# Kernel optimization log

Hardware: AMD Instinct MI355X
Metric: run time of the kernel (lower is better)

## Reference

```python
import math
import jax, jax.numpy as jnp
import numpy as np

FACTOR = 5
N_HEADS = 8


def setup_inputs() -> dict:
    key = jax.random.key(0)
    ks = jax.random.split(key, 9)
    B, S, D = 4, 8192, 512
    s = 0.02
    x = jax.random.normal(ks[0], (B, S, D), jnp.float32)
    Wq = jax.random.normal(ks[1], (D, D), jnp.float32) * s
    bq = jax.random.normal(ks[2], (D,), jnp.float32) * s
    Wk = jax.random.normal(ks[3], (D, D), jnp.float32) * s
    bk = jax.random.normal(ks[4], (D,), jnp.float32) * s
    Wv = jax.random.normal(ks[5], (D, D), jnp.float32) * s
    bv = jax.random.normal(ks[6], (D,), jnp.float32) * s
    Wo = jax.random.normal(ks[7], (D, D), jnp.float32) * s
    bo = jax.random.normal(ks[8], (D,), jnp.float32) * s
    return {"x": x, "Wq": Wq, "bq": bq, "Wk": Wk, "bk": bk,
            "Wv": Wv, "bv": bv, "Wo": Wo, "bo": bo}


def reference(x, Wq, bq, Wk, bk, Wv, bv, Wo, bo):
    B, S, D = x.shape
    H = N_HEADS
    hd = D // H
    scale = hd ** -0.5

    def proj(W, b):
        # [B,S,D] -> [B,H,S,hd]
        return (x @ W + b).reshape(B, S, H, hd).transpose(0, 2, 1, 3)

    q = proj(Wq, bq)
    k = proj(Wk, bk)
    v = proj(Wv, bv)

    # number of "active" queries: O(log S)
    sampled = max(1, min(S, int(FACTOR * math.log(S + 1))))

    sparsity = jnp.sum(q * q, axis=-1)                    # [B,H,S]
    top_idx = jax.lax.top_k(sparsity, sampled)[1]         # [B,H,u]

    sel_q = jnp.take_along_axis(q, top_idx[..., None], axis=2)  # [B,H,u,hd]
    scores = jnp.einsum('bhud,bhsd->bhus', sel_q, k) * scale     # [B,H,u,S]
    attn = jax.nn.softmax(scores, axis=-1)
    sel_ctx = jnp.einsum('bhus,bhsd->bhud', attn, v)             # [B,H,u,hd]

    # default context = mean of values; overwrite rows of selected queries
    ctx = jnp.broadcast_to(v.mean(axis=2, keepdims=True), (B, H, S, hd))
    bi = jnp.arange(B)[:, None, None]
    hi = jnp.arange(H)[None, :, None]
    ctx = ctx.at[bi, hi, top_idx].set(sel_ctx)                   # scatter [B,H,S,hd]

    ctx = ctx.transpose(0, 2, 1, 3).reshape(B, S, D)
    return ctx @ Wo + bo
```

## Files before the change

### kernel.cpp

```cpp
#include <hip/hip_runtime.h>
#include <hip/hip_fp16.h>
#include <math.h>

#define B_ 4
#define S_ 8192
#define D_ 512
#define H_ 8
#define U_ 45
#define NCHUNK 16

typedef unsigned short ushortT;
typedef __attribute__((ext_vector_type(8))) _Float16 half8;
typedef __attribute__((ext_vector_type(4))) float f32x4;

__device__ __forceinline__ ushortT f2h(float f) {
    return __half_as_ushort(__float2half(f));
}
__device__ __forceinline__ float h2f(ushortT u) {
    return __half2float(__ushort_as_half(u));
}

__device__ __forceinline__ void gload_lds16(const ushortT* g, ushortT* l) {
    __builtin_amdgcn_global_load_lds(
        (const __attribute__((address_space(1))) void*)g,
        (__attribute__((address_space(3))) void*)l,
        16, 0, 0);
}

__global__ __launch_bounds__(256) void prep_kernel(
    const float* __restrict__ X, ushortT* __restrict__ Xf,
    const float* __restrict__ Wq, const float* __restrict__ Wk,
    const float* __restrict__ Wv,
    ushortT* __restrict__ WqT, ushortT* __restrict__ WkT,
    ushortT* __restrict__ WvT,
    float* __restrict__ vsum, float* __restrict__ outbase)
{
    __shared__ float t[32][33];
    const int bx = blockIdx.x;
    if (bx < 8192) {
        if (bx == 0) {
            float4 z = {0.f, 0.f, 0.f, 0.f};
            *(float4*)&vsum[threadIdx.x * 8]        = z;
            *(float4*)&vsum[threadIdx.x * 8 + 4]    = z;
            *(float4*)&outbase[threadIdx.x * 8]     = z;
            *(float4*)&outbase[threadIdx.x * 8 + 4] = z;
        }
        size_t i = ((size_t)bx * 256 + threadIdx.x) * 8;
        float4 a = *(const float4*)(X + i);
        float4 b = *(const float4*)(X + i + 4);
        *(ushort4*)(Xf + i)     = make_ushort4(f2h(a.x), f2h(a.y), f2h(a.z), f2h(a.w));
        *(ushort4*)(Xf + i + 4) = make_ushort4(f2h(b.x), f2h(b.y), f2h(b.z), f2h(b.w));
    } else {
        const int idx = bx - 8192;
        const int z = idx >> 8, rem = idx & 255;
        const int r0 = (rem >> 4) * 32, c0 = (rem & 15) * 32;
        const float* W = (z == 0) ? Wq : (z == 1) ? Wk : Wv;
        ushortT* O = (z == 0) ? WqT : (z == 1) ? WkT : WvT;
        const int tx = threadIdx.x & 31, ty4 = (threadIdx.x >> 5) * 4;
#pragma unroll
        for (int i = 0; i < 4; ++i)
            t[ty4 + i][tx] = W[(size_t)(r0 + ty4 + i) * 512 + c0 + tx];
        __syncthreads();
#pragma unroll
        for (int i = 0; i < 4; ++i)
            O[(size_t)(c0 + ty4 + i) * 512 + r0 + tx] = f2h(t[tx][ty4 + i]);
    }
}

__global__ __launch_bounds__(256, 2) void qkv_mfma(
    const ushortT* __restrict__ Xf,
    const ushortT* __restrict__ WqT, const ushortT* __restrict__ WkT,
    const ushortT* __restrict__ WvT,
    const float* __restrict__ bq, const float* __restrict__ bk,
    const float* __restrict__ bv,
    ushortT* __restrict__ Qbuf, ushortT* __restrict__ Kbuf,
    ushortT* __restrict__ VT,
    float* __restrict__ sparsity, float* __restrict__ vsum)
{
    __shared__ ushortT lds[2 * 128 * 64];
    ushortT* As = lds;
    ushortT* Bs = lds + 8192;

    const int tid  = threadIdx.x;
    const int w    = tid >> 6, lane = tid & 63;
    const int quad = lane >> 4, c16 = lane & 15;
    const int wr   = w >> 1,  wc  = w & 1;
    const int mat  = blockIdx.y >> 2;
    const int nt   = blockIdx.y & 3;
    const int m0   = blockIdx.x * 128;
    const int n0   = nt * 128;

    const int srowL = lane >> 3;
    const int slc   = (((lane & 7) - (srowL & 7)) & 7) * 8;
    const int rrot  = c16 & 7;

    const ushortT* Ag = (mat == 2) ? WvT : Xf;
    const ushortT* Bg = (mat == 0) ? WqT : (mat == 1) ? WkT : Xf;
    const int arow0 = (mat == 2) ? n0 : m0;
    const int brow0 = (mat == 2) ? m0 : n0;

    f32x4 acc[4][4];
#pragma unroll
    for (int i = 0; i < 4; ++i)
#pragma unroll
        for (int j = 0; j < 4; ++j) acc[i][j] = (f32x4){0.f, 0.f, 0.f, 0.f};

    for (int k0 = 0; k0 < 512; k0 += 64) {
        __syncthreads();
#pragma unroll
        for (int c = 0; c < 4; ++c) {
            const int R = c * 32 + w * 8 + srowL;
            const int lbase = c * 2048 + w * 512;
            gload_lds16(Ag + (size_t)(arow0 + R) * 512 + k0 + slc, As + lbase);
            gload_lds16(Bg + (size_t)(brow0 + R) * 512 + k0 + slc, Bs + lbase);
        }
        __syncthreads();
#pragma unroll
        for (int kk = 0; kk < 2; ++kk) {
            const int phk = (((kk * 4 + quad) + rrot) & 7) * 8;
            half8 af[4], bf[4];
#pragma unroll
            for (int i = 0; i < 4; ++i) {
                af[i] = *(const half8*)&As[(wr * 64 + i * 16 + c16) * 64 + phk];
                bf[i] = *(const half8*)&Bs[(wc * 64 + i * 16 + c16) * 64 + phk];
            }
#pragma unroll
            for (int i = 0; i < 4; ++i)
#pragma unroll
                for (int j = 0; j < 4; ++j)
                    acc[i][j] = __builtin_amdgcn_mfma_f32_16x16x32_f16(af[i], bf[j], acc[i][j], 0, 0, 0);
        }
    }

    if (mat == 0) {
        const int b = m0 >> 13;
        const int head = (n0 + wc * 64) >> 6;
        float bb[4];
#pragma unroll
        for (int j = 0; j < 4; ++j) bb[j] = bq[n0 + wc * 64 + j * 16 + c16];
        ushortT* qbase = Qbuf + ((size_t)(b * 8 + head) * 8192) * 64;
#pragma unroll
        for (int i = 0; i < 4; ++i)
#pragma unroll
            for (int r = 0; r < 4; ++r) {
                const int s = (m0 & 8191) + wr * 64 + i * 16 + quad * 4 + r;
                float p = 0.f;
#pragma unroll
                for (int j = 0; j < 4; ++j) {
                    float v = acc[i][j][r] + bb[j];
                    qbase[(size_t)s * 64 + j * 16 + c16] = f2h(v);
                    p = fmaf(v, v, p);
                }
                p += __shfl_xor(p, 1);
                p += __shfl_xor(p, 2);
                p += __shfl_xor(p, 4);
                p += __shfl_xor(p, 8);
                if (c16 == 0)
                    sparsity[((size_t)b * H_ + head) * S_ + s] = p;
            }
    } else if (mat == 1) {
        const int b = m0 >> 13;
        const int head = (n0 + wc * 64) >> 6;
        float bb[4];
#pragma unroll
        for (int j = 0; j < 4; ++j) bb[j] = bk[n0 + wc * 64 + j * 16 + c16];
        ushortT* kbase = Kbuf + ((size_t)(b * 8 + head) * 8192) * 64;
#pragma unroll
        for (int i = 0; i < 4; ++i)
#pragma unroll
            for (int r = 0; r < 4; ++r) {
                const int s = (m0 & 8191) + wr * 64 + i * 16 + quad * 4 + r;
#pragma unroll
                for (int j = 0; j < 4; ++j)
                    kbase[(size_t)s * 64 + j * 16 + c16] = f2h(acc[i][j][r] + bb[j]);
            }
    } else {
        const int b = m0 >> 13;
        const int sbase = (m0 & 8191) + wc * 64;
#pragma unroll
        for (int i = 0; i < 4; ++i)
#pragma unroll
            for (int r = 0; r < 4; ++r) {
                const int dcol = n0 + wr * 64 + i * 16 + quad * 4 + r;
                const int head = dcol >> 6, dd = dcol & 63;
                const float biasv = bv[dcol];
                ushortT* vrow = VT + ((size_t)(b * 8 + head) * 64 + dd) * 8192;
                float vsa = 0.f;
#pragma unroll
                for (int j = 0; j < 4; ++j) {
                    float v = acc[i][j][r] + biasv;
                    vrow[sbase + j * 16 + c16] = f2h(v);
                    vsa += v;
                }
                vsa += __shfl_xor(vsa, 1);
                vsa += __shfl_xor(vsa, 2);
                vsa += __shfl_xor(vsa, 4);
                vsa += __shfl_xor(vsa, 8);
                if (c16 == 0) atomicAdd(&vsum[b * 512 + dcol], vsa);
            }
    }
}

__global__ __launch_bounds__(256) void topk_kernel(
    const float* __restrict__ sparsity, int* __restrict__ topidx,
    const float* __restrict__ vsum, const float* __restrict__ Wo,
    const float* __restrict__ bo, float* __restrict__ outbase)
{
    __shared__ unsigned vals[S_];
    __shared__ unsigned hist[8][256];
    __shared__ int ssum[256];
    __shared__ unsigned prefix_s;
    __shared__ int need_s;
    __shared__ int cnt_gt_s, cnt_eq_s;
    __shared__ int eqidx[64];
    const int tid = threadIdx.x;

    if (blockIdx.x >= 32) {
        const int idx = blockIdx.x - 32;
        const int b = idx >> 3, ks = (idx & 7) >> 1, dh = idx & 1;
        const int d = dh * 256 + tid;
        float acc = (ks == 0) ? bo[d] : 0.f;
        const int r0 = ks * 128;
        for (int r = r0; r < r0 + 128; ++r) {
            float mv = vsum[b * 512 + r] * (1.0f / S_);
            acc = fmaf(mv, Wo[(size_t)r * 512 + d], acc);
        }
        atomicAdd(&outbase[b * 512 + d], acc);
        return;
    }

    const int bh = blockIdx.x;
    const unsigned* sp = (const unsigned*)(sparsity + (size_t)bh * S_);
    for (int i = tid; i < S_; i += 256) vals[i] = sp[i];

    unsigned prefix = 0;
    int need = U_;
    const int rep = tid & 7;
    for (int level = 0; level < 4; ++level) {
        const int shift = 24 - level * 8;
#pragma unroll
        for (int r = 0; r < 8; ++r) hist[r][tid] = 0;
        __syncthreads();
        const unsigned pmask = (level == 0) ? 0u : (0xFFFFFFFFu << (shift + 8));
        for (int i = tid; i < S_; i += 256) {
            unsigned v = vals[i];
            if ((v & pmask) == prefix)
                atomicAdd(&hist[rep][(v >> shift) & 255], 1u);
        }
        __syncthreads();
        int bs = 0;
#pragma unroll
        for (int r = 0; r < 8; ++r) bs += (int)hist[r][tid];
        ssum[tid] = bs;
        __syncthreads();
        for (int off = 1; off < 256; off <<= 1) {
            int add = (tid + off < 256) ? ssum[tid + off] : 0;
            __syncthreads();
            ssum[tid] += add;
            __syncthreads();
        }
        int snext = (tid == 255) ? 0 : ssum[tid + 1];
        if (ssum[tid] >= need && snext < need) {
            prefix_s = prefix | ((unsigned)tid << shift);
            need_s = need - snext;
        }
        __syncthreads();
        prefix = prefix_s;
        need = need_s;
        __syncthreads();
    }
    const unsigned T = prefix;
    if (tid == 0) { cnt_gt_s = 0; cnt_eq_s = 0; }
    __syncthreads();
    for (int i = tid; i < S_; i += 256) {
        unsigned v = vals[i];
        if (v > T) {
            int p = atomicAdd(&cnt_gt_s, 1);
            topidx[bh * U_ + p] = i;
        } else if (v == T) {
            int p = atomicAdd(&cnt_eq_s, 1);
            if (p < 64) eqidx[p] = i;
        }
    }
    __syncthreads();
    if (tid == 0) {
        int rem = U_ - cnt_gt_s;
        int n = cnt_eq_s < 64 ? cnt_eq_s : 64;
        for (int a = 0; a < rem; ++a) {
            int best = 1 << 30, bj = 0;
            for (int j = 0; j < n; ++j)
                if (eqidx[j] < best) { best = eqidx[j]; bj = j; }
            topidx[bh * U_ + cnt_gt_s + a] = best;
            eqidx[bj] = 1 << 30;
        }
    }
}

__global__ __launch_bounds__(256, 2) void attn_mfma(
    const ushortT* __restrict__ Qbuf, const ushortT* __restrict__ Kbuf,
    const ushortT* __restrict__ VT, const int* __restrict__ topidx,
    float* __restrict__ pl, float* __restrict__ pacc)
{
    __shared__ float sc[48 * 132];
    __shared__ ushortT Qb[48 * 72];

    const int tid = threadIdx.x;
    const int w = tid >> 6, lane = tid & 63;
    const int quad = lane >> 4, c16 = lane & 15;
    const int bh = blockIdx.y;
    const int s_base = blockIdx.x * 512;

    for (int i = tid; i < 48 * 64; i += 256) {
        int q = i >> 6, d = i & 63;
        float v = 0.f;
        if (q < U_) {
            int s = topidx[bh * U_ + q];
            v = h2f(Qbuf[((size_t)bh * 8192 + s) * 64 + d]) * 0.125f;
        }
        Qb[q * 72 + d] = f2h(v);
    }

    f32x4 O[3];
#pragma unroll
    for (int mt = 0; mt < 3; ++mt) O[mt] = (f32x4){0.f, 0.f, 0.f, 0.f};
    float lacc[12];
#pragma unroll
    for (int qi = 0; qi < 12; ++qi) lacc[qi] = 0.f;

    __syncthreads();

    half8 qa[3][2];
#pragma unroll
    for (int mt = 0; mt < 3; ++mt)
#pragma unroll
        for (int kk = 0; kk < 2; ++kk)
            qa[mt][kk] = *(const half8*)&Qb[(mt * 16 + c16) * 72 + kk * 32 + quad * 8];

    const ushortT* kb  = Kbuf + (size_t)bh * 8192 * 64;
    const ushortT* vtb = VT + ((size_t)bh * 64 + w * 16 + c16) * 8192;

    for (int ci = 0; ci < 4; ++ci) {
        const int s0 = s_base + ci * 128;

        half8 kf[2][2];
#pragma unroll
        for (int nt2 = 0; nt2 < 2; ++nt2)
#pragma unroll
            for (int kk = 0; kk < 2; ++kk)
                kf[nt2][kk] = *(const half8*)&kb[
                    (size_t)(s0 + w * 32 + nt2 * 16 + c16) * 64 + kk * 32 + quad * 8];
        f32x4 sacc[3][2];
#pragma unroll
        for (int mt = 0; mt < 3; ++mt)
#pragma unroll
            for (int nt2 = 0; nt2 < 2; ++nt2) {
                sacc[mt][nt2] = (f32x4){0.f, 0.f, 0.f, 0.f};
#pragma unroll
                for (int kk = 0; kk < 2; ++kk)
                    sacc[mt][nt2] = __builtin_amdgcn_mfma_f32_16x16x32_f16(
                        qa[mt][kk], kf[nt2][kk], sacc[mt][nt2], 0, 0, 0);
            }
#pragma unroll
        for (int mt = 0; mt < 3; ++mt)
#pragma unroll
            for (int nt2 = 0; nt2 < 2; ++nt2)
#pragma unroll
                for (int r = 0; r < 4; ++r)
                    sc[(mt * 16 + quad * 4 + r) * 132 + w * 32 + nt2 * 16 + c16] =
                        sacc[mt][nt2][r];
        __syncthreads();

        half8 vb[4];
#pragma unroll
        for (int kk = 0; kk < 4; ++kk)
            vb[kk] = *(const half8*)&vtb[s0 + kk * 32 + quad * 8];

#pragma unroll
        for (int qi = 0; qi < 12; ++qi) {
            const int q = w * 12 + qi;
            float x0 = sc[q * 132 + lane];
            float x1 = sc[q * 132 + 64 + lane];
            ushortT u0 = f2h(__expf(x0));
            ushortT u1 = f2h(__expf(x1));
            lacc[qi] += h2f(u0) + h2f(u1);
            ushortT* pr = (ushortT*)&sc[q * 132];
            pr[lane] = u0;
            pr[lane + 64] = u1;
        }
        __syncthreads();

#pragma unroll
        for (int mt = 0; mt < 3; ++mt)
#pragma unroll
            for (int kk = 0; kk < 4; ++kk) {
                half8 pa = *(const half8*)((const ushortT*)sc +
                    (size_t)(mt * 16 + c16) * 264 + kk * 32 + quad * 8);
                O[mt] = __builtin_amdgcn_mfma_f32_16x16x32_f16(pa, vb[kk], O[mt], 0, 0, 0);
            }
        __syncthreads();
    }

#pragma unroll
    for (int mt = 0; mt < 3; ++mt)
#pragma unroll
        for (int r = 0; r < 4; ++r) {
            const int q = mt * 16 + quad * 4 + r;
            if (q < U_)
                pacc[(((size_t)bh * NCHUNK + blockIdx.x) * U_ + q) * 64 + w * 16 + c16] =
                    O[mt][r];
        }
#pragma unroll
    for (int qi = 0; qi < 12; ++qi) {
        const int q = w * 12 + qi;
        float ssum = lacc[qi];
#pragma unroll
        for (int off = 1; off < 64; off <<= 1) ssum += __shfl_xor(ssum, off);
        if (lane == 0 && q < U_)
            pl[((size_t)bh * NCHUNK + blockIdx.x) * U_ + q] = ssum;
    }
}

__global__ __launch_bounds__(256) void fill_kernel(
    const float* __restrict__ outbase, float* __restrict__ out)
{
    size_t gid = (size_t)blockIdx.x * 256 + threadIdx.x;
    size_t e0 = gid * 4;
    int b = (int)(e0 >> 22);
    int col = (int)(e0 & 511);
    float4 v = *(const float4*)&outbase[b * 512 + col];
    *(float4*)&out[e0] = v;
}

__global__ __launch_bounds__(512) void corr_out_kernel(
    const float* __restrict__ pl, const float* __restrict__ pacc,
    const float* __restrict__ vsum, const float* __restrict__ Wo,
    const int* __restrict__ topidx, float* __restrict__ out)
{
    __shared__ float corrS[64];
    const int q = blockIdx.x, bh = blockIdx.y;
    const int b = bh >> 3, h = bh & 7, tid = threadIdx.x;
    if (tid < 64) {
        float L = 0.f, a = 0.f;
        for (int c = 0; c < NCHUNK; ++c) {
            L += pl[((size_t)bh * NCHUNK + c) * U_ + q];
            a += pacc[(((size_t)bh * NCHUNK + c) * U_ + q) * 64 + tid];
        }
        corrS[tid] = a / L - vsum[b * 512 + h * 64 + tid] * (1.0f / S_);
    }
    __syncthreads();
    const int s = topidx[bh * U_ + q];
    const int d = tid;
    float delta = 0.f;
#pragma unroll
    for (int r = 0; r < 64; ++r)
        delta = fmaf(corrS[r], Wo[(size_t)(h * 64 + r) * 512 + d], delta);
    atomicAdd(&out[((size_t)b * S_ + s) * 512 + d], delta);
}

extern "C" void kernel_launch(void* const* d_in, const int* in_sizes, int n_in,
                              void* d_out, int out_size, void* d_ws, size_t ws_size,
                              hipStream_t stream)
{
    const float* X  = (const float*)d_in[0];
    const float* Wq = (const float*)d_in[1];
    const float* bq = (const float*)d_in[2];
    const float* Wk = (const float*)d_in[3];
    const float* bk = (const float*)d_in[4];
    const float* Wv = (const float*)d_in[5];
    const float* bv = (const float*)d_in[6];
    const float* Wo = (const float*)d_in[7];
    const float* bo = (const float*)d_in[8];
    float* out = (float*)d_out;

    char* ws = (char*)d_ws;
    size_t off = 0;
    auto alloc = [&](size_t bytes) {
        void* p = ws + off;
        off = (off + bytes + 255) & ~(size_t)255;
        return p;
    };
    ushortT* Xf   = (ushortT*)alloc((size_t)B_ * S_ * D_ * 2);
    ushortT* Qbuf = (ushortT*)alloc((size_t)B_ * S_ * D_ * 2);
    ushortT* Kbuf = (ushortT*)alloc((size_t)B_ * S_ * D_ * 2);
    ushortT* VT   = (ushortT*)alloc((size_t)B_ * S_ * D_ * 2);
    ushortT* WqT  = (ushortT*)alloc((size_t)D_ * D_ * 2);
    ushortT* WkT  = (ushortT*)alloc((size_t)D_ * D_ * 2);
    ushortT* WvT  = (ushortT*)alloc((size_t)D_ * D_ * 2);
    float* sparsity = (float*)alloc((size_t)B_ * H_ * S_ * 4);
    int*   topidx   = (int*)alloc((size_t)B_ * H_ * U_ * 4);
    float* pl       = (float*)alloc((size_t)B_ * H_ * NCHUNK * U_ * 4);
    float* pacc     = (float*)alloc((size_t)B_ * H_ * NCHUNK * U_ * 64 * 4);
    float* vsum     = (float*)alloc((size_t)B_ * 512 * 4);
    float* outbase  = (float*)alloc((size_t)B_ * 512 * 4);

    prep_kernel<<<8960, 256, 0, stream>>>(X, Xf, Wq, Wk, Wv, WqT, WkT, WvT,
                                          vsum, outbase);
    qkv_mfma<<<dim3(256, 12), 256, 0, stream>>>(Xf, WqT, WkT, WvT,
                                                bq, bk, bv, Qbuf, Kbuf, VT,
                                                sparsity, vsum);
    topk_kernel<<<64, 256, 0, stream>>>(sparsity, topidx, vsum, Wo, bo, outbase);
    attn_mfma<<<dim3(NCHUNK, B_ * H_), 256, 0, stream>>>(Qbuf, Kbuf, VT, topidx,
                                                         pl, pacc);
    fill_kernel<<<(B_ * S_ * D_ / 4 + 255) / 256, 256, 0, stream>>>(outbase, out);
    corr_out_kernel<<<dim3(U_, B_ * H_), 512, 0, stream>>>(pl, pacc, vsum, Wo,
                                                           topidx, out);
}
```

Before: 282.9 us.

## Overlap top-k selection with K/V projection and fold mean-output into attention launch

Splits the QKV projection into a Q-only launch followed by a K/V launch that also carries 32 extra blocks running the radix top-k on sparsity. The top-k then overlaps with the K/V GEMM instead of running as its own serial kernel. The mean-value times Wo blocks move into the attention launch as an extra grid column. Top-k now reads sparsity straight from global memory rather than caching it in LDS, and it shares the GEMM kernel's LDS and launch bounds.

```diff
diff --git a/kernel.cpp b/kernel.cpp
--- a/kernel.cpp
+++ b/kernel.cpp
@@ -75,18 +75,98 @@
     const float* __restrict__ bv,
     ushortT* __restrict__ Qbuf, ushortT* __restrict__ Kbuf,
     ushortT* __restrict__ VT,
-    float* __restrict__ sparsity, float* __restrict__ vsum)
+    float* __restrict__ sparsity, float* __restrict__ vsum,
+    int* __restrict__ topidx, int mode)
 {
     __shared__ ushortT lds[2 * 128 * 64];
     ushortT* As = lds;
     ushortT* Bs = lds + 8192;
 
     const int tid  = threadIdx.x;
+
+    if (mode == 1 && blockIdx.y == 8) {
+        if (blockIdx.x >= 32) return;
+        char* sm = (char*)lds;
+        unsigned (*hist)[256] = (unsigned (*)[256])sm;
+        int* ssum            = (int*)(sm + 8192);
+        unsigned* prefix_s   = (unsigned*)(sm + 9216);
+        int* need_s          = (int*)(sm + 9220);
+        int* cnt_gt_s        = (int*)(sm + 9224);
+        int* cnt_eq_s        = (int*)(sm + 9228);
+        int* eqidx           = (int*)(sm + 9232);
+
+        const int bh = blockIdx.x;
+        const unsigned* sp = (const unsigned*)(sparsity + (size_t)bh * S_);
+
+        unsigned prefix = 0;
+        int need = U_;
+        const int rep = tid & 7;
+        for (int level = 0; level < 4; ++level) {
+            const int shift = 24 - level * 8;
+#pragma unroll
+            for (int r = 0; r < 8; ++r) hist[r][tid] = 0;
+            __syncthreads();
+            const unsigned pmask = (level == 0) ? 0u : (0xFFFFFFFFu << (shift + 8));
+            for (int i = tid; i < S_; i += 256) {
+                unsigned v = sp[i];
+                if ((v & pmask) == prefix)
+                    atomicAdd(&hist[rep][(v >> shift) & 255], 1u);
+            }
+            __syncthreads();
+            int bs = 0;
+#pragma unroll
+            for (int r = 0; r < 8; ++r) bs += (int)hist[r][tid];
+            ssum[tid] = bs;
+            __syncthreads();
+            for (int off = 1; off < 256; off <<= 1) {
+                int add = (tid + off < 256) ? ssum[tid + off] : 0;
+                __syncthreads();
+                ssum[tid] += add;
+                __syncthreads();
+            }
+            int snext = (tid == 255) ? 0 : ssum[tid + 1];
+            if (ssum[tid] >= need && snext < need) {
+                *prefix_s = prefix | ((unsigned)tid << shift);
+                *need_s = need - snext;
+            }
+            __syncthreads();
+            prefix = *prefix_s;
+            need = *need_s;
+            __syncthreads();
+        }
+        const unsigned T = prefix;
+        if (tid == 0) { *cnt_gt_s = 0; *cnt_eq_s = 0; }
+        __syncthreads();
+        for (int i = tid; i < S_; i += 256) {
+            unsigned v = sp[i];
+            if (v > T) {
+                int p = atomicAdd(cnt_gt_s, 1);
+                topidx[bh * U_ + p] = i;
+            } else if (v == T) {
+                int p = atomicAdd(cnt_eq_s, 1);
+                if (p < 64) eqidx[p] = i;
+            }
+        }
+        __syncthreads();
+        if (tid == 0) {
+            int rem = U_ - *cnt_gt_s;
+            int n = *cnt_eq_s < 64 ? *cnt_eq_s : 64;
+            for (int a = 0; a < rem; ++a) {
+                int best = 1 << 30, bj = 0;
+                for (int j = 0; j < n; ++j)
+                    if (eqidx[j] < best) { best = eqidx[j]; bj = j; }
+                topidx[bh * U_ + *cnt_gt_s + a] = best;
+                eqidx[bj] = 1 << 30;
+            }
+        }
+        return;
+    }
+
     const int w    = tid >> 6, lane = tid & 63;
     const int quad = lane >> 4, c16 = lane & 15;
     const int wr   = w >> 1,  wc  = w & 1;
-    const int mat  = blockIdx.y >> 2;
-    const int nt   = blockIdx.y & 3;
+    const int mat  = (mode == 0) ? 0 : 1 + (blockIdx.y >> 2);
+    const int nt   = (mode == 0) ? blockIdx.y : (blockIdx.y & 3);
     const int m0   = blockIdx.x * 128;
     const int n0   = nt * 128;
 
@@ -201,22 +281,20 @@
     }
 }
 
-__global__ __launch_bounds__(256) void topk_kernel(
-    const float* __restrict__ sparsity, int* __restrict__ topidx,
+__global__ __launch_bounds__(256, 2) void attn_mfma(
+    const ushortT* __restrict__ Qbuf, const ushortT* __restrict__ Kbuf,
+    const ushortT* __restrict__ VT, const int* __restrict__ topidx,
+    float* __restrict__ pl, float* __restrict__ pacc,
     const float* __restrict__ vsum, const float* __restrict__ Wo,
     const float* __restrict__ bo, float* __restrict__ outbase)
 {
-    __shared__ unsigned vals[S_];
-    __shared__ unsigned hist[8][256];
-    __shared__ int ssum[256];
-    __shared__ unsigned prefix_s;
-    __shared__ int need_s;
-    __shared__ int cnt_gt_s, cnt_eq_s;
-    __shared__ int eqidx[64];
+    __shared__ float sc[48 * 132];
+    __shared__ ushortT Qb[48 * 72];
+
     const int tid = threadIdx.x;
 
-    if (blockIdx.x >= 32) {
-        const int idx = blockIdx.x - 32;
+    if (blockIdx.x == 16) {
+        const int idx = blockIdx.y;
         const int b = idx >> 3, ks = (idx & 7) >> 1, dh = idx & 1;
         const int d = dh * 256 + tid;
         float acc = (ks == 0) ? bo[d] : 0.f;
@@ -229,82 +307,6 @@
         return;
     }
 
-    const int bh = blockIdx.x;
-    const unsigned* sp = (const unsigned*)(sparsity + (size_t)bh * S_);
-    for (int i = tid; i < S_; i += 256) vals[i] = sp[i];
-
-    unsigned prefix = 0;
-    int need = U_;
-    const int rep = tid & 7;
-    for (int level = 0; level < 4; ++level) {
-        const int shift = 24 - level * 8;
-#pragma unroll
-        for (int r = 0; r < 8; ++r) hist[r][tid] = 0;
-        __syncthreads();
-        const unsigned pmask = (level == 0) ? 0u : (0xFFFFFFFFu << (shift + 8));
-        for (int i = tid; i < S_; i += 256) {
-            unsigned v = vals[i];
-            if ((v & pmask) == prefix)
-                atomicAdd(&hist[rep][(v >> shift) & 255], 1u);
-        }
-        __syncthreads();
-        int bs = 0;
-#pragma unroll
-        for (int r = 0; r < 8; ++r) bs += (int)hist[r][tid];
-        ssum[tid] = bs;
-        __syncthreads();
-        for (int off = 1; off < 256; off <<= 1) {
-            int add = (tid + off < 256) ? ssum[tid + off] : 0;
-            __syncthreads();
-            ssum[tid] += add;
-            __syncthreads();
-        }
-        int snext = (tid == 255) ? 0 : ssum[tid + 1];
-        if (ssum[tid] >= need && snext < need) {
-            prefix_s = prefix | ((unsigned)tid << shift);
-            need_s = need - snext;
-        }
-        __syncthreads();
-        prefix = prefix_s;
-        need = need_s;
-        __syncthreads();
-    }
-    const unsigned T = prefix;
-    if (tid == 0) { cnt_gt_s = 0; cnt_eq_s = 0; }
-    __syncthreads();
-    for (int i = tid; i < S_; i += 256) {
-        unsigned v = vals[i];
-        if (v > T) {
-            int p = atomicAdd(&cnt_gt_s, 1);
-            topidx[bh * U_ + p] = i;
-        } else if (v == T) {
-            int p = atomicAdd(&cnt_eq_s, 1);
-            if (p < 64) eqidx[p] = i;
-        }
-    }
-    __syncthreads();
-    if (tid == 0) {
-        int rem = U_ - cnt_gt_s;
-        int n = cnt_eq_s < 64 ? cnt_eq_s : 64;
-        for (int a = 0; a < rem; ++a) {
-            int best = 1 << 30, bj = 0;
-            for (int j = 0; j < n; ++j)
-                if (eqidx[j] < best) { best = eqidx[j]; bj = j; }
-            topidx[bh * U_ + cnt_gt_s + a] = best;
-            eqidx[bj] = 1 << 30;
-        }
-    }
-}
-
-__global__ __launch_bounds__(256, 2) void attn_mfma(
-    const ushortT* __restrict__ Qbuf, const ushortT* __restrict__ Kbuf,
-    const ushortT* __restrict__ VT, const int* __restrict__ topidx,
-    float* __restrict__ pl, float* __restrict__ pacc)
-{
-    __shared__ float sc[48 * 132];
-    __shared__ ushortT Qb[48 * 72];
-
-    const int tid = threadIdx.x;
     const int w = tid >> 6, lane = tid & 63;
     const int quad = lane >> 4, c16 = lane & 15;
     const int bh = blockIdx.y;
@@ -495,12 +497,14 @@
 
     prep_kernel<<<8960, 256, 0, stream>>>(X, Xf, Wq, Wk, Wv, WqT, WkT, WvT,
                                           vsum, outbase);
-    qkv_mfma<<<dim3(256, 12), 256, 0, stream>>>(Xf, WqT, WkT, WvT,
-                                                bq, bk, bv, Qbuf, Kbuf, VT,
-                                                sparsity, vsum);
-    topk_kernel<<<64, 256, 0, stream>>>(sparsity, topidx, vsum, Wo, bo, outbase);
-    attn_mfma<<<dim3(NCHUNK, B_ * H_), 256, 0, stream>>>(Qbuf, Kbuf, VT, topidx,
-                                                         pl, pacc);
+    qkv_mfma<<<dim3(256, 4), 256, 0, stream>>>(Xf, WqT, WkT, WvT,
+                                               bq, bk, bv, Qbuf, Kbuf, VT,
+                                               sparsity, vsum, topidx, 0);
+    qkv_mfma<<<dim3(256, 9), 256, 0, stream>>>(Xf, WqT, WkT, WvT,
+                                               bq, bk, bv, Qbuf, Kbuf, VT,
+                                               sparsity, vsum, topidx, 1);
+    attn_mfma<<<dim3(NCHUNK + 1, B_ * H_), 256, 0, stream>>>(
+        Qbuf, Kbuf, VT, topidx, pl, pacc, vsum, Wo, bo, outbase);
     fill_kernel<<<(B_ * S_ * D_ / 4 + 255) / 256, 256, 0, stream>>>(outbase, out);
     corr_out_kernel<<<dim3(U_, B_ * H_), 512, 0, stream>>>(pl, pacc, vsum, Wo,
                                                            topidx, out);
```

Measured after the change: 299.1 us. 1.06x slower.

## Fuse Q and K projections into one block sharing the X tile

Applied to the files above, without the earlier changes.

The QKV GEMM now launches 512-thread blocks over a 6-row grid. Blocks for Q/K load one X tile and both WqT and WkT tiles, so X is loaded once for both projections, with half the waves computing Q and half K. V blocks cover 256 output columns against a 128-row X tile, which reuses the X tile across more weight rows. LDS use grows to three 16 KB tiles, and the larger blocks may lower occupancy or change scheduling.

```diff
diff --git a/kernel.cpp b/kernel.cpp
--- a/kernel.cpp
+++ b/kernel.cpp
@@ -67,7 +67,7 @@
     }
 }
 
-__global__ __launch_bounds__(256, 2) void qkv_mfma(
+__global__ __launch_bounds__(512, 2) void qkv_mfma(
     const ushortT* __restrict__ Xf,
     const ushortT* __restrict__ WqT, const ushortT* __restrict__ WkT,
     const ushortT* __restrict__ WvT,
@@ -77,27 +77,25 @@
     ushortT* __restrict__ VT,
     float* __restrict__ sparsity, float* __restrict__ vsum)
 {
-    __shared__ ushortT lds[2 * 128 * 64];
-    ushortT* As = lds;
-    ushortT* Bs = lds + 8192;
+    __shared__ ushortT lds[3 * 128 * 64];
 
     const int tid  = threadIdx.x;
     const int w    = tid >> 6, lane = tid & 63;
     const int quad = lane >> 4, c16 = lane & 15;
-    const int wr   = w >> 1,  wc  = w & 1;
-    const int mat  = blockIdx.y >> 2;
-    const int nt   = blockIdx.y & 3;
+    const bool fusedQK = (blockIdx.y < 4);
+    const int stream = w >> 2;
+    const int aw   = fusedQK ? ((w >> 1) & 1) : (w >> 1);
+    const int bw   = w & 1;
     const int m0   = blockIdx.x * 128;
-    const int n0   = nt * 128;
+    const int n0   = fusedQK ? (blockIdx.y * 128) : ((blockIdx.y - 4) * 256);
 
     const int srowL = lane >> 3;
     const int slc   = (((lane & 7) - (srowL & 7)) & 7) * 8;
     const int rrot  = c16 & 7;
 
-    const ushortT* Ag = (mat == 2) ? WvT : Xf;
-    const ushortT* Bg = (mat == 0) ? WqT : (mat == 1) ? WkT : Xf;
-    const int arow0 = (mat == 2) ? n0 : m0;
-    const int brow0 = (mat == 2) ? m0 : n0;
+    const ushortT* Brd = fusedQK ? (lds + 8192 + stream * 8192) : (lds + 16384);
+    const int awBase = aw * 64;
+    const int bwBase = bw * 64;
 
     f32x4 acc[4][4];
 #pragma unroll
@@ -107,12 +105,28 @@
 
     for (int k0 = 0; k0 < 512; k0 += 64) {
         __syncthreads();
-#pragma unroll
-        for (int c = 0; c < 4; ++c) {
-            const int R = c * 32 + w * 8 + srowL;
-            const int lbase = c * 2048 + w * 512;
-            gload_lds16(Ag + (size_t)(arow0 + R) * 512 + k0 + slc, As + lbase);
-            gload_lds16(Bg + (size_t)(brow0 + R) * 512 + k0 + slc, Bs + lbase);
+        if (fusedQK) {
+#pragma unroll
+            for (int c = 0; c < 2; ++c) {
+                const int R  = c * 64 + w * 8 + srowL;
+                const int lb = c * 4096 + w * 512;
+                gload_lds16(Xf  + (size_t)(m0 + R) * 512 + k0 + slc, lds + lb);
+                gload_lds16(WqT + (size_t)(n0 + R) * 512 + k0 + slc, lds + 8192 + lb);
+                gload_lds16(WkT + (size_t)(n0 + R) * 512 + k0 + slc, lds + 16384 + lb);
+            }
+        } else {
+#pragma unroll
+            for (int c = 0; c < 4; ++c) {
+                const int R = c * 64 + w * 8 + srowL;
+                gload_lds16(WvT + (size_t)(n0 + R) * 512 + k0 + slc,
+                            lds + c * 4096 + w * 512);
+            }
+#pragma unroll
+            for (int c = 0; c < 2; ++c) {
+                const int R = c * 64 + w * 8 + srowL;
+                gload_lds16(Xf + (size_t)(m0 + R) * 512 + k0 + slc,
+                            lds + 16384 + c * 4096 + w * 512);
+            }
         }
         __syncthreads();
 #pragma unroll
@@ -121,8 +135,8 @@
             half8 af[4], bf[4];
 #pragma unroll
             for (int i = 0; i < 4; ++i) {
-                af[i] = *(const half8*)&As[(wr * 64 + i * 16 + c16) * 64 + phk];
-                bf[i] = *(const half8*)&Bs[(wc * 64 + i * 16 + c16) * 64 + phk];
+                af[i] = *(const half8*)&lds[(awBase + i * 16 + c16) * 64 + phk];
+                bf[i] = *(const half8*)&Brd[(bwBase + i * 16 + c16) * 64 + phk];
             }
 #pragma unroll
             for (int i = 0; i < 4; ++i)
@@ -132,18 +146,18 @@
         }
     }
 
-    if (mat == 0) {
-        const int b = m0 >> 13;
-        const int head = (n0 + wc * 64) >> 6;
+    const int b = m0 >> 13;
+    if (fusedQK && stream == 0) {
+        const int head = (n0 + bw * 64) >> 6;
         float bb[4];
 #pragma unroll
-        for (int j = 0; j < 4; ++j) bb[j] = bq[n0 + wc * 64 + j * 16 + c16];
+        for (int j = 0; j < 4; ++j) bb[j] = bq[n0 + bw * 64 + j * 16 + c16];
         ushortT* qbase = Qbuf + ((size_t)(b * 8 + head) * 8192) * 64;
 #pragma unroll
         for (int i = 0; i < 4; ++i)
 #pragma unroll
             for (int r = 0; r < 4; ++r) {
-                const int s = (m0 & 8191) + wr * 64 + i * 16 + quad * 4 + r;
+                const int s = (m0 & 8191) + awBase + i * 16 + quad * 4 + r;
                 float p = 0.f;
 #pragma unroll
                 for (int j = 0; j < 4; ++j) {
@@ -158,30 +172,28 @@
                 if (c16 == 0)
                     sparsity[((size_t)b * H_ + head) * S_ + s] = p;
             }
-    } else if (mat == 1) {
-        const int b = m0 >> 13;
-        const int head = (n0 + wc * 64) >> 6;
+    } else if (fusedQK) {
+        const int head = (n0 + bw * 64) >> 6;
         float bb[4];
 #pragma unroll
-        for (int j = 0; j < 4; ++j) bb[j] = bk[n0 + wc * 64 + j * 16 + c16];
+        for (int j = 0; j < 4; ++j) bb[j] = bk[n0 + bw * 64 + j * 16 + c16];
         ushortT* kbase = Kbuf + ((size_t)(b * 8 + head) * 8192) * 64;
 #pragma unroll
         for (int i = 0; i < 4; ++i)
 #pragma unroll
             for (int r = 0; r < 4; ++r) {
-                const int s = (m0 & 8191) + wr * 64 + i * 16 + quad * 4 + r;
+                const int s = (m0 & 8191) + awBase + i * 16 + quad * 4 + r;
 #pragma unroll
                 for (int j = 0; j < 4; ++j)
                     kbase[(size_t)s * 64 + j * 16 + c16] = f2h(acc[i][j][r] + bb[j]);
             }
     } else {
-        const int b = m0 >> 13;
-        const int sbase = (m0 & 8191) + wc * 64;
+        const int sbase = (m0 & 8191) + bwBase;
 #pragma unroll
         for (int i = 0; i < 4; ++i)
 #pragma unroll
             for (int r = 0; r < 4; ++r) {
-                const int dcol = n0 + wr * 64 + i * 16 + quad * 4 + r;
+                const int dcol = n0 + awBase + i * 16 + quad * 4 + r;
                 const int head = dcol >> 6, dd = dcol & 63;
                 const float biasv = bv[dcol];
                 ushortT* vrow = VT + ((size_t)(b * 8 + head) * 64 + dd) * 8192;
@@ -495,9 +507,9 @@
 
     prep_kernel<<<8960, 256, 0, stream>>>(X, Xf, Wq, Wk, Wv, WqT, WkT, WvT,
                                           vsum, outbase);
-    qkv_mfma<<<dim3(256, 12), 256, 0, stream>>>(Xf, WqT, WkT, WvT,
-                                                bq, bk, bv, Qbuf, Kbuf, VT,
-                                                sparsity, vsum);
+    qkv_mfma<<<dim3(256, 6), 512, 0, stream>>>(Xf, WqT, WkT, WvT,
+                                               bq, bk, bv, Qbuf, Kbuf, VT,
+                                               sparsity, vsum);
     topk_kernel<<<64, 256, 0, stream>>>(sparsity, topidx, vsum, Wo, bo, outbase);
     attn_mfma<<<dim3(NCHUNK, B_ * H_), 256, 0, stream>>>(Qbuf, Kbuf, VT, topidx,
                                                          pl, pacc);
```

Result: no change. 279.6 us (-1.1%).
